# Kernel tuning notes

Measured on AMD Instinct MI355X. Metric: run time of the kernel, lower is better.

Reference implementation:

```python
import jax, jax.numpy as jnp
import numpy as np

B, D, N, H, K = 4, 1024, 4096, 16, 128
DH = D // H  # per-head dim (note: torch view splits D as (DH, H) in that order)
BN_EPS = 1e-3


def conv1(x, w, b):
    # 1x1 Conv1d == channel matmul: x [B,Cin,N], w [Cout,Cin], b [Cout]
    return jnp.einsum('oi,bin->bon', w, x) + b[None, :, None]


def setup_inputs() -> dict:
    key = jax.random.key(0)
    ks = jax.random.split(key, 16)
    s = 0.02
    proj_std = 1.0 / np.sqrt(K)  # init_() uniform(-1/sqrt(k), 1/sqrt(k))
    return {
        'x': jax.random.normal(ks[0], (B, D, N), jnp.float32),
        'source': jax.random.normal(ks[1], (B, D, N), jnp.float32),
        'to_q_w': jax.random.normal(ks[2], (D, D), jnp.float32) * s,
        'to_q_b': jnp.zeros((D,), jnp.float32),
        'to_k_w': jax.random.normal(ks[3], (D, D), jnp.float32) * s,
        'to_k_b': jnp.zeros((D,), jnp.float32),
        'proj_k': jax.random.uniform(ks[4], (N, K), jnp.float32, -proj_std, proj_std),
        'merge_w': jax.random.normal(ks[5], (D, D), jnp.float32) * s,
        'merge_b': jnp.zeros((D,), jnp.float32),
        'mlp_w1': jax.random.normal(ks[6], (2 * D, 2 * D), jnp.float32) * s,
        'mlp_b1': jnp.zeros((2 * D,), jnp.float32),
        'bn_gamma': jnp.ones((2 * D,), jnp.float32),
        'bn_beta': jnp.zeros((2 * D,), jnp.float32),
        'bn_mean': jnp.zeros((2 * D,), jnp.float32),
        'bn_var': jnp.ones((2 * D,), jnp.float32),
        'mlp_w2': jax.random.normal(ks[7], (D, 2 * D), jnp.float32) * s,
        'mlp_b2': jnp.zeros((D,), jnp.float32),
    }


def reference(x, source, to_q_w, to_q_b, to_k_w, to_k_b, proj_k, merge_w, merge_b,
              mlp_w1, mlp_b1, bn_gamma, bn_beta, bn_mean, bn_var, mlp_w2, mlp_b2):
    b = x.shape[0]
    q = conv1(x, to_q_w, to_q_b)          # [B,D,N]
    k = conv1(source, to_k_w, to_k_b)     # [B,D,M]
    v = k                                  # share_kv=True
    # Linformer sequence-length reduction: M -> K (proj_v == proj_k when shared)
    k = jnp.einsum('bdm,mk->bdk', k, proj_k)   # [B,D,K]
    v = jnp.einsum('bdm,mk->bdk', v, proj_k)   # [B,D,K]
    # torch .view(B, dim, heads, -1): channel axis split as (DH, H)
    qh = q.reshape(b, DH, H, N)
    kh = k.reshape(b, DH, H, K)
    vh = v.reshape(b, DH, H, K)
    scores = jnp.einsum('bdhn,bdhk->bhnk', qh, kh) / (DH ** 0.5)
    prob = jax.nn.softmax(scores, axis=-1)      # [B,H,N,K], small K
    msg = jnp.einsum('bhnk,bdhk->bdhn', prob, vh).reshape(b, D, N)
    msg = conv1(msg, merge_w, merge_b)
    # MLP([2D, 2D, D]): conv -> BN(eval, eps=1e-3) -> ReLU -> conv
    h = jnp.concatenate([x, msg], axis=1)       # [B,2D,N]
    h = conv1(h, mlp_w1, mlp_b1)
    h = bn_gamma[None, :, None] * (h - bn_mean[None, :, None]) \
        * jax.lax.rsqrt(bn_var + BN_EPS)[None, :, None] + bn_beta[None, :, None]
    h = jax.nn.relu(h)
    return conv1(h, mlp_w2, mlp_b2)             # [B,D,N]
```

## Files before the change

kernel.cpp:

```cpp
#include <hip/hip_runtime.h>
#include <stdint.h>

typedef __bf16 bf16x8 __attribute__((ext_vector_type(8)));
typedef float f32x4 __attribute__((ext_vector_type(4)));

__device__ __forceinline__ unsigned short f2bf(float f) {
    union { float f; uint32_t i; } v;
    v.f = f;
    uint32_t x = v.i;
    return (unsigned short)((x + 0x7FFFu + ((x >> 16) & 1u)) >> 16);
}

typedef __attribute__((address_space(3))) unsigned int lds_u32;
typedef __attribute__((address_space(1))) const unsigned int glob_u32;
__device__ __forceinline__ void gld16(const unsigned short* g, unsigned short* l) {
    __builtin_amdgcn_global_load_lds((glob_u32*)g, (lds_u32*)l, 16, 0, 0);
}

__global__ __launch_bounds__(256) void prep_weights(
    const float* __restrict__ Wq, const float* __restrict__ Wk,
    const float* __restrict__ Wm, const float* __restrict__ W1,
    const float* __restrict__ W2, const float* __restrict__ bq,
    const float* __restrict__ bk,
    unsigned short* __restrict__ wqb, unsigned short* __restrict__ wkb,
    unsigned short* __restrict__ wmb, unsigned short* __restrict__ w1b,
    unsigned short* __restrict__ w2b, float* __restrict__ bqp,
    float* __restrict__ bkp)
{
    const int b = blockIdx.x, t = threadIdx.x;
    if (b < 2048) {
        const float* in = (b < 1024) ? Wq : Wk;
        unsigned short* out = (b < 1024) ? wqb : wkb;
        const int i = ((b & 1023) * 256 + t) * 4;
        const int row = i >> 10, col = i & 1023;
        const float4 v = *(const float4*)(in + ((row & 63) * 16 + (row >> 6)) * 1024 + col);
        out[i + 0] = f2bf(v.x); out[i + 1] = f2bf(v.y);
        out[i + 2] = f2bf(v.z); out[i + 3] = f2bf(v.w);
    } else if (b < 3072) {
        const int i = ((b - 2048) * 256 + t) * 4;
        const int row = i >> 10, c0 = i & 1023;
        const float* r = Wm + (size_t)row * 1024;
#pragma unroll
        for (int j = 0; j < 4; ++j) {
            const int c = c0 + j;
            wmb[i + j] = f2bf(r[(c & 63) * 16 + (c >> 6)]);
        }
    } else if (b < 7168) {
        const int i = ((b - 3072) * 256 + t) * 4;
        const float4 v = *(const float4*)(W1 + i);
        w1b[i + 0] = f2bf(v.x); w1b[i + 1] = f2bf(v.y);
        w1b[i + 2] = f2bf(v.z); w1b[i + 3] = f2bf(v.w);
    } else if (b < 9216) {
        const int i = ((b - 7168) * 256 + t) * 4;
        const float4 v = *(const float4*)(W2 + i);
        w2b[i + 0] = f2bf(v.x); w2b[i + 1] = f2bf(v.y);
        w2b[i + 2] = f2bf(v.z); w2b[i + 3] = f2bf(v.w);
    } else {
        const int o = (b - 9216) * 256 + t;
        const int src = (o & 63) * 16 + (o >> 6);
        bqp[o] = bq[src];
        bkp[o] = bk[src];
    }
}

__global__ __launch_bounds__(256) void cvt_transpose(
    const float* __restrict__ in, unsigned short* __restrict__ out,
    int R, int C)
{
    __shared__ unsigned short tile[32][33];
    const size_t bo = (size_t)blockIdx.z * R * C;
    const int c0 = blockIdx.x * 32, r0 = blockIdx.y * 32;
    const int tx = threadIdx.x & 31, ty = threadIdx.x >> 5;
#pragma unroll
    for (int i = 0; i < 4; ++i)
        tile[ty + i * 8][tx] = f2bf(in[bo + (size_t)(r0 + ty + i * 8) * C + (c0 + tx)]);
    __syncthreads();
#pragma unroll
    for (int i = 0; i < 4; ++i)
        out[bo + (size_t)(c0 + ty + i * 8) * R + (r0 + tx)] = tile[tx][ty + i * 8];
}

__global__ __launch_bounds__(256) void cvt_transpose_xs(
    const float* __restrict__ x, const float* __restrict__ s,
    unsigned short* __restrict__ xt, unsigned short* __restrict__ st)
{
    __shared__ unsigned short tile[32][33];
    const int z = blockIdx.z;
    const float* in = (z < 4) ? x : s;
    unsigned short* out = (z < 4) ? xt : st;
    const size_t bo = (size_t)(z & 3) * 1024 * 4096;
    const int c0 = blockIdx.x * 32, r0 = blockIdx.y * 32;
    const int tx = threadIdx.x & 31, ty = threadIdx.x >> 5;
#pragma unroll
    for (int i = 0; i < 4; ++i)
        tile[ty + i * 8][tx] = f2bf(in[bo + (size_t)(r0 + ty + i * 8) * 4096 + (c0 + tx)]);
    __syncthreads();
#pragma unroll
    for (int i = 0; i < 4; ++i)
        out[bo + (size_t)(c0 + ty + i * 8) * 1024 + (r0 + tx)] = tile[tx][ty + i * 8];
}

template<int LDA, int LDB, int LDC, int KD, int SPLIT, bool CONCAT>
__global__ __launch_bounds__(256) void gemm_bt(
    const unsigned short* __restrict__ A,
    const unsigned short* __restrict__ A2, int K1,
    const unsigned short* __restrict__ BT,
    unsigned short* __restrict__ C, float* __restrict__ Cf,
    long long strideA, long long strideB, long long strideC,
    const float* __restrict__ bias_m,
    const float* __restrict__ bias_n,
    const float* __restrict__ bn_g,
    const float* __restrict__ bn_b,
    const float* __restrict__ bn_mu,
    const float* __restrict__ bn_var)
{
    constexpr int KPB = KD / SPLIT;
    __shared__ __align__(16) unsigned short As[128 * 64];
    __shared__ __align__(16) unsigned short Bs[128 * 64];

    const int z = blockIdx.z;
    const int batch = z / SPLIT;
    const int kbase = (z % SPLIT) * KPB;
    const int m0 = blockIdx.y * 128, n0 = blockIdx.x * 128;
    const unsigned short* Ab  = A + (size_t)batch * strideA;
    const unsigned short* A2b = CONCAT ? A2 + (size_t)batch * strideA
                                       : (const unsigned short*)0;
    const unsigned short* Bb = BT + (size_t)batch * strideB;

    const int t = threadIdx.x;
    const int lane = t & 63, wid = t >> 6;
    const int wm = wid >> 1, wn = wid & 1;
    const int r16 = lane & 15, quad = lane >> 4;

    f32x4 acc[4][4];
    const f32x4 zf = {0.f, 0.f, 0.f, 0.f};
#pragma unroll
    for (int i = 0; i < 4; ++i)
#pragma unroll
        for (int j = 0; j < 4; ++j) acc[i][j] = zf;

    for (int kt = kbase; kt < kbase + KPB; kt += 64) {
        const unsigned short* Asrc = Ab;
        int kk = kt;
        if (CONCAT && kt >= K1) { Asrc = A2b; kk = kt - K1; }
#pragma unroll
        for (int i = 0; i < 4; ++i) {
            const int p = i * 256 + t;
            const int row = p >> 3, slot = p & 7;
            const int kc = (slot ^ (row & 7)) * 8;
            gld16(&Asrc[(size_t)(m0 + row) * LDA + kk + kc], &As[p * 8]);
            gld16(&Bb[(size_t)(n0 + row) * LDB + kt + kc], &Bs[p * 8]);
        }
        __syncthreads();
#pragma unroll
        for (int s = 0; s < 2; ++s) {
            bf16x8 af[4], bfb[4];
#pragma unroll
            for (int i = 0; i < 4; ++i) {
                const int ra = wm * 64 + i * 16 + r16;
                const int rb = wn * 64 + i * 16 + r16;
                af[i]  = *(const bf16x8*)&As[(ra * 8 + ((s * 4 + quad) ^ (ra & 7))) * 8];
                bfb[i] = *(const bf16x8*)&Bs[(rb * 8 + ((s * 4 + quad) ^ (rb & 7))) * 8];
            }
#pragma unroll
            for (int mi = 0; mi < 4; ++mi)
#pragma unroll
                for (int ni = 0; ni < 4; ++ni)
                    acc[mi][ni] = __builtin_amdgcn_mfma_f32_16x16x32_bf16(
                        af[mi], bfb[ni], acc[mi][ni], 0, 0, 0);
        }
        __syncthreads();
    }

    unsigned short* Cb = C ? C + (size_t)z * strideC : (unsigned short*)0;
    float* Cfb = Cf ? Cf + (size_t)z * strideC : (float*)0;
    const bool has_bn = (bn_g != 0);
#pragma unroll
    for (int ni = 0; ni < 4; ++ni) {
        const int gn = n0 + wn * 64 + ni * 16 + r16;
        const float addn = bias_n ? bias_n[gn] : 0.f;
        float g = 1.f, bb = 0.f, mu = 0.f, rstd = 1.f;
        if (has_bn) {
            g = bn_g[gn]; bb = bn_b[gn]; mu = bn_mu[gn];
            rstd = rsqrtf(bn_var[gn] + 1e-3f);
        }
#pragma unroll
        for (int mi = 0; mi < 4; ++mi) {
            const int gm0 = m0 + wm * 64 + mi * 16 + quad * 4;
#pragma unroll
            for (int r = 0; r < 4; ++r) {
                float v = acc[mi][ni][r] + addn;
                if (bias_m) v += bias_m[gm0 + r];
                if (has_bn) { v = g * (v - mu) * rstd + bb; v = fmaxf(v, 0.f); }
                const size_t idx = (size_t)(gm0 + r) * LDC + gn;
                if (Cfb) Cfb[idx] = v;
                else     Cb[idx]  = f2bf(v);
            }
        }
    }
}

#define BAR   __builtin_amdgcn_s_barrier()
#define LGKM0 asm volatile("s_waitcnt lgkmcnt(0)" ::: "memory")
#define PRIO1 __builtin_amdgcn_s_setprio(1)
#define PRIO0 __builtin_amdgcn_s_setprio(0)

#define ST_A(dst, kt, i0, i1) do {                                          \
    const unsigned short* S_ = Ab; long long kk_ = (kt);                    \
    if (CONCAT && (kt) >= K1) { S_ = A2b; kk_ = (kt) - K1; }                \
    gld16(&S_[offA[i0] + kk_], (dst) + po[i0]);                             \
    gld16(&S_[offA[i1] + kk_], (dst) + po[i1]); } while (0)

#define ST_B(dst, kt, i0, i1) do {                                          \
    gld16(&Bb[offB[i0] + (kt)], (dst) + po[i0]);                            \
    gld16(&Bb[offB[i1] + (kt)], (dst) + po[i1]); } while (0)

#define RD_A(mh, AC) do {                                                   \
    _Pragma("unroll") for (int mi = 0; mi < 4; ++mi) {                      \
        const int ra = wm * 128 + (mh) * 64 + mi * 16 + r16;                \
        _Pragma("unroll") for (int ks = 0; ks < 2; ++ks) {                  \
            const int c_ = ks * 4 + quad;                                   \
            a[mi][ks] = *(const bf16x8*)&(AC)[(ra * 8 + (c_ ^ (ra & 7))) * 8]; \
        } } } while (0)

#define RD_B(np, BC) do {                                                   \
    _Pragma("unroll") for (int i = 0; i < 2; ++i) {                         \
        const int rb = wn * 64 + ((np) * 2 + i) * 16 + r16;                 \
        _Pragma("unroll") for (int ks = 0; ks < 2; ++ks) {                  \
            const int c_ = ks * 4 + quad;                                   \
            b[(np) * 2 + i][ks] = *(const bf16x8*)&(BC)[(rb * 8 + (c_ ^ (rb & 7))) * 8]; \
        } } } while (0)

#define MFMA_PH(mh, np) do {                                                \
    _Pragma("unroll") for (int mi = 0; mi < 4; ++mi)                        \
    _Pragma("unroll") for (int i = 0; i < 2; ++i)                           \
    _Pragma("unroll") for (int ks = 0; ks < 2; ++ks)                        \
        acc[(mh) * 4 + mi][(np) * 2 + i] =                                  \
            __builtin_amdgcn_mfma_f32_16x16x32_bf16(                        \
                a[mi][ks], b[(np) * 2 + i][ks],                             \
                acc[(mh) * 4 + mi][(np) * 2 + i], 0, 0, 0); } while (0)

#define TILE_BODY(XV, AC, BC, AN) do {                                      \
    const int kt1_ = ((XV) + 1) * 64, kt2_ = ((XV) + 2) * 64;               \
    const bool g1_ = ((XV) + 1) < nt, g2_ = ((XV) + 2) < nt;                \
       \
    RD_A(0, AC); RD_B(0, BC);                                               \
    if (g1_) ST_A(AN, kt1_, 1, 3);                                          \
    asm volatile("s_waitcnt lgkmcnt(8)" ::: "memory");                      \
    BAR; LGKM0; PRIO1; MFMA_PH(0, 0); PRIO0; BAR;                           \
                                  \
    RD_B(1, BC);                                                            \
    BAR; LGKM0; PRIO1; MFMA_PH(0, 1); PRIO0; BAR;                           \
         \
    RD_A(1, AC);                                                            \
    if (g2_) { ST_B(BC, kt2_, 0, 1); ST_B(BC, kt2_, 2, 3); }                \
    BAR; LGKM0; PRIO1; MFMA_PH(1, 1); PRIO0; BAR;                           \
             \
    if (g2_) { ST_A(AC, kt2_, 0, 2);                                        \
               asm volatile("s_waitcnt vmcnt(6)" ::: "memory"); }           \
    else     { asm volatile("s_waitcnt vmcnt(0)" ::: "memory"); }           \
    BAR; LGKM0; PRIO1; MFMA_PH(1, 0); PRIO0; BAR;                           \
} while (0)

template<int LDA, int LDB, int LDC, int KD, bool CONCAT>
__global__ __launch_bounds__(512, 2) void gemm256(
    const unsigned short* __restrict__ A,
    const unsigned short* __restrict__ A2, int K1,
    const unsigned short* __restrict__ BT,
    unsigned short* __restrict__ C, float* __restrict__ Cf,
    long long strideA, long long strideB, long long strideC,
    const float* __restrict__ bias_m,
    const float* __restrict__ bias_n,
    const float* __restrict__ bn_g,
    const float* __restrict__ bn_b,
    const float* __restrict__ bn_mu,
    const float* __restrict__ bn_var)
{
    static_assert(KD % 128 == 0, "nt must be even");
    constexpr int nt = KD / 64;
    constexpr int TILE = 256 * 64;
    __shared__ __align__(16) unsigned short As0[TILE];
    __shared__ __align__(16) unsigned short As1[TILE];
    __shared__ __align__(16) unsigned short Bs0[TILE];
    __shared__ __align__(16) unsigned short Bs1[TILE];

    const int batch = blockIdx.z;
    const int gx = gridDim.x;
    const int nwg = gx * gridDim.y;
    int flat = blockIdx.y * gx + blockIdx.x;
    flat = (flat & 7) * (nwg >> 3) + (flat >> 3);
    const int n0 = (flat % gx) * 256;
    const int m0 = (flat / gx) * 256;

    const unsigned short* Ab  = A + (size_t)batch * strideA;
    const unsigned short* A2b = CONCAT ? A2 + (size_t)batch * strideA
                                       : (const unsigned short*)0;
    const unsigned short* Bb  = BT + (size_t)batch * strideB;

    const int t = threadIdx.x;
    const int lane = t & 63, wid = t >> 6;
    const int wm = wid >> 2, wn = wid & 3;
    const int r16 = lane & 15, quad = lane >> 4;

    long long offA[4], offB[4];
    int po[4];
#pragma unroll
    for (int i = 0; i < 4; ++i) {
        const int p = i * 512 + t, row = p >> 3;
        const int kc = ((p & 7) ^ (row & 7)) * 8;
        po[i] = p * 8;
        offA[i] = (long long)(m0 + row) * LDA + kc;
        offB[i] = (long long)(n0 + row) * LDB + kc;
    }

    f32x4 acc[8][4];
    const f32x4 zf = {0.f, 0.f, 0.f, 0.f};
#pragma unroll
    for (int i = 0; i < 8; ++i)
#pragma unroll
        for (int j = 0; j < 4; ++j) acc[i][j] = zf;

    bf16x8 a[4][2], b[4][2];

    ST_A(As0, 0, 0, 2);
    ST_B(Bs0, 0, 0, 1);
    ST_B(Bs0, 0, 2, 3);
    ST_A(As0, 0, 1, 3);
    ST_B(Bs1, 64, 0, 1);
    ST_B(Bs1, 64, 2, 3);
    ST_A(As1, 64, 0, 2);
    asm volatile("s_waitcnt vmcnt(6)" ::: "memory");
    BAR;

#pragma unroll 1
    for (int X2 = 0; X2 < nt; X2 += 2) {
        TILE_BODY(X2,     As0, Bs0, As1);
        TILE_BODY(X2 + 1, As1, Bs1, As0);
    }

    unsigned short* Cb = C ? C + (size_t)batch * strideC : (unsigned short*)0;
    float* Cfb = Cf ? Cf + (size_t)batch * strideC : (float*)0;
    const bool has_bn = (bn_g != 0);

    float addn4[4], g4[4], b4[4], mu4[4], rs4[4];
#pragma unroll
    for (int ni = 0; ni < 4; ++ni) {
        const int gn = n0 + wn * 64 + ni * 16 + r16;
        addn4[ni] = bias_n ? bias_n[gn] : 0.f;
        if (has_bn) {
            g4[ni] = bn_g[gn]; b4[ni] = bn_b[gn]; mu4[ni] = bn_mu[gn];
            rs4[ni] = rsqrtf(bn_var[gn] + 1e-3f);
        }
    }
#pragma unroll
    for (int mi = 0; mi < 8; ++mi) {
        const int gm0 = m0 + wm * 128 + mi * 16 + quad * 4;
#pragma unroll
        for (int r = 0; r < 4; ++r) {
            const float bm_ = bias_m ? bias_m[gm0 + r] : 0.f;
            const size_t rowb = (size_t)(gm0 + r) * LDC + n0 + wn * 64 + r16;
#pragma unroll
            for (int ni = 0; ni < 4; ++ni) {
                float v = acc[mi][ni][r] + addn4[ni] + bm_;
                if (has_bn) {
                    v = g4[ni] * (v - mu4[ni]) * rs4[ni] + b4[ni];
                    v = fmaxf(v, 0.f);
                }
                if (Cfb) Cfb[rowb + ni * 16] = v;
                else     Cb[rowb + ni * 16]  = f2bf(v);
            }
        }
    }
}

#undef TILE_BODY
#undef MFMA_PH
#undef RD_B
#undef RD_A
#undef ST_B
#undef ST_A
#undef PRIO0
#undef PRIO1
#undef LGKM0
#undef BAR

__global__ __launch_bounds__(256) void reduce_kp(
    const float* __restrict__ acc, unsigned short* __restrict__ kpb)
{
    const int j = (blockIdx.x * 256 + threadIdx.x) * 4;
    const int b = j >> 17, jj = j & 131071;
    const float* base = acc + (size_t)b * 8 * 131072 + jj;
    float4 s = *(const float4*)base;
#pragma unroll
    for (int p = 1; p < 8; ++p) {
        const float4 v = *(const float4*)(base + (size_t)p * 131072);
        s.x += v.x; s.y += v.y; s.z += v.z; s.w += v.w;
    }
    kpb[j + 0] = f2bf(s.x); kpb[j + 1] = f2bf(s.y);
    kpb[j + 2] = f2bf(s.z); kpb[j + 3] = f2bf(s.w);
}

__global__ __launch_bounds__(256) void attn_fused(
    const unsigned short* __restrict__ qT,
    const unsigned short* __restrict__ kp,
    unsigned short* __restrict__ msgT)
{
    constexpr int QS = 72, KS = 72, VS = 136, PS = 136;
    __shared__ __align__(16) unsigned short QKP[128 * QS + 128 * KS];
    __shared__ __align__(16) unsigned short Vs[64 * VS];
    unsigned short* Qs = QKP;
    unsigned short* Ks = QKP + 128 * QS;
    unsigned short* Ps = QKP;

    const int t = threadIdx.x;
    const int lane = t & 63, w = t >> 6;
    const int r16 = lane & 15, quad = lane >> 4;
    const int h = blockIdx.y, n0 = blockIdx.x * 128;
    const size_t b = blockIdx.z;

    const unsigned short* qbase = qT + (b * 4096 + n0) * 1024 + h * 64;
    const unsigned short* kbase = kp + (b * 1024 + h * 64) * 128;

#pragma unroll
    for (int i = 0; i < 4; ++i) {
        const int c = i * 256 + t;
        const int n = c >> 3, dh0 = (c & 7) * 8;
        *(int4*)&Qs[n * QS + dh0] = *(const int4*)&qbase[(size_t)n * 1024 + dh0];
    }
#pragma unroll
    for (int i = 0; i < 4; ++i) {
        const int c = i * 256 + t;
        const int kkq = c & 3, dh = (c >> 2) & 63, kkh = c >> 8;
        const int kk0 = kkh * 32 + kkq * 8;
        const bf16x8 v = *(const bf16x8*)&kbase[(size_t)dh * 128 + kk0];
        *(bf16x8*)&Vs[dh * VS + kk0] = v;
        const unsigned short* vs = (const unsigned short*)&v;
#pragma unroll
        for (int j = 0; j < 8; ++j) Ks[(kk0 + j) * KS + dh] = vs[j];
    }
    __syncthreads();

    f32x4 S[2][8];
    const f32x4 zf = {0.f, 0.f, 0.f, 0.f};
#pragma unroll
    for (int mi = 0; mi < 2; ++mi)
#pragma unroll
        for (int ni = 0; ni < 8; ++ni) S[mi][ni] = zf;

    bf16x8 aq[2][2];
#pragma unroll
    for (int mi = 0; mi < 2; ++mi)
#pragma unroll
        for (int ks = 0; ks < 2; ++ks)
            aq[mi][ks] = *(const bf16x8*)&Qs[(w * 32 + mi * 16 + r16) * QS + ks * 32 + quad * 8];
#pragma unroll
    for (int ni = 0; ni < 8; ++ni) {
        const bf16x8 b0 = *(const bf16x8*)&Ks[(ni * 16 + r16) * KS + quad * 8];
        const bf16x8 b1 = *(const bf16x8*)&Ks[(ni * 16 + r16) * KS + 32 + quad * 8];
#pragma unroll
        for (int mi = 0; mi < 2; ++mi) {
            S[mi][ni] = __builtin_amdgcn_mfma_f32_16x16x32_bf16(aq[mi][0], b0, S[mi][ni], 0, 0, 0);
            S[mi][ni] = __builtin_amdgcn_mfma_f32_16x16x32_bf16(aq[mi][1], b1, S[mi][ni], 0, 0, 0);
        }
    }

    __syncthreads();

    float linv[2][4];
#pragma unroll
    for (int mi = 0; mi < 2; ++mi) {
        float e[8][4];
        float rs0 = 0.f, rs1 = 0.f, rs2 = 0.f, rs3 = 0.f;
#pragma unroll
        for (int ni = 0; ni < 8; ++ni) {
            e[ni][0] = __expf(S[mi][ni][0] * 0.125f); rs0 += e[ni][0];
            e[ni][1] = __expf(S[mi][ni][1] * 0.125f); rs1 += e[ni][1];
            e[ni][2] = __expf(S[mi][ni][2] * 0.125f); rs2 += e[ni][2];
            e[ni][3] = __expf(S[mi][ni][3] * 0.125f); rs3 += e[ni][3];
        }
        float rs[4] = {rs0, rs1, rs2, rs3};
#pragma unroll
        for (int r = 0; r < 4; ++r) {
            float s = rs[r];
            s += __shfl_xor(s, 1); s += __shfl_xor(s, 2);
            s += __shfl_xor(s, 4); s += __shfl_xor(s, 8);
            linv[mi][r] = 1.f / s;
        }
#pragma unroll
        for (int ni = 0; ni < 8; ++ni)
#pragma unroll
            for (int r = 0; r < 4; ++r)
                Ps[(w * 32 + mi * 16 + quad * 4 + r) * PS + ni * 16 + r16] = f2bf(e[ni][r]);
    }
    __syncthreads();

    f32x4 O[2][4];
#pragma unroll
    for (int mi = 0; mi < 2; ++mi)
#pragma unroll
        for (int ni = 0; ni < 4; ++ni) O[mi][ni] = zf;

    bf16x8 ap[2][4];
#pragma unroll
    for (int mi = 0; mi < 2; ++mi)
#pragma unroll
        for (int ks = 0; ks < 4; ++ks)
            ap[mi][ks] = *(const bf16x8*)&Ps[(w * 32 + mi * 16 + r16) * PS + ks * 32 + quad * 8];
#pragma unroll
    for (int ni = 0; ni < 4; ++ni)
#pragma unroll
        for (int ks = 0; ks < 4; ++ks) {
            const bf16x8 bv = *(const bf16x8*)&Vs[(ni * 16 + r16) * VS + ks * 32 + quad * 8];
#pragma unroll
            for (int mi = 0; mi < 2; ++mi)
                O[mi][ni] = __builtin_amdgcn_mfma_f32_16x16x32_bf16(ap[mi][ks], bv, O[mi][ni], 0, 0, 0);
        }

    unsigned short* ob = msgT + (b * 4096 + n0) * 1024 + h * 64;
#pragma unroll
    for (int mi = 0; mi < 2; ++mi)
#pragma unroll
        for (int ni = 0; ni < 4; ++ni)
#pragma unroll
            for (int r = 0; r < 4; ++r)
                ob[(size_t)(w * 32 + mi * 16 + quad * 4 + r) * 1024 + ni * 16 + r16] =
                    f2bf(O[mi][ni][r] * linv[mi][r]);
}

extern "C" void kernel_launch(void* const* d_in, const int* in_sizes, int n_in,
                              void* d_out, int out_size, void* d_ws, size_t ws_size,
                              hipStream_t stream)
{
    (void)in_sizes; (void)n_in; (void)out_size; (void)ws_size;
    const float* x    = (const float*)d_in[0];
    const float* srcp = (const float*)d_in[1];
    const float* Wq   = (const float*)d_in[2];
    const float* bq   = (const float*)d_in[3];
    const float* Wk   = (const float*)d_in[4];
    const float* bk   = (const float*)d_in[5];
    const float* proj = (const float*)d_in[6];
    const float* Wm   = (const float*)d_in[7];
    const float* bm   = (const float*)d_in[8];
    const float* W1   = (const float*)d_in[9];
    const float* b1   = (const float*)d_in[10];
    const float* gam  = (const float*)d_in[11];
    const float* bet  = (const float*)d_in[12];
    const float* mu   = (const float*)d_in[13];
    const float* var  = (const float*)d_in[14];
    const float* W2   = (const float*)d_in[15];
    const float* b2   = (const float*)d_in[16];
    float* out = (float*)d_out;
    unsigned short* ws = (unsigned short*)d_ws;

    const long long E = 16777216LL;
    unsigned short* xt  = ws;
    unsigned short* st  = xt + E;
    unsigned short* qt  = st + E;
    unsigned short* kc  = qt + E;
    unsigned short* ht  = kc + E;
    unsigned short* pT  = ht + 2 * E;
    unsigned short* kpb = pT + 524288;
    unsigned short* wqb = kpb + 524288;
    unsigned short* wkb = wqb + 1048576;
    unsigned short* wmb = wkb + 1048576;
    unsigned short* w1b = wmb + 1048576;
    unsigned short* w2b = w1b + 4194304;
    float* bqp = (float*)(w2b + 2097152);
    float* bkp = bqp + 1024;
    float* kpacc = (float*)ht;

    cvt_transpose_xs<<<dim3(128, 32, 8), 256, 0, stream>>>(x, srcp, xt, st);
    cvt_transpose<<<dim3(4, 128, 1), 256, 0, stream>>>(proj, pT, 4096, 128);
    prep_weights<<<9220, 256, 0, stream>>>(Wq, Wk, Wm, W1, W2, bq, bk,
                                           wqb, wkb, wmb, w1b, w2b, bqp, bkp);

    gemm256<1024, 1024, 1024, 1024, false><<<dim3(4, 16, 4), 512, 0, stream>>>(
        xt, nullptr, 1024, wqb, qt, nullptr,
        4096LL * 1024, 0LL, 4096LL * 1024, nullptr, bqp,
        nullptr, nullptr, nullptr, nullptr);
    gemm256<1024, 1024, 4096, 1024, false><<<dim3(16, 4, 4), 512, 0, stream>>>(
        wkb, nullptr, 1024, st, kc, nullptr,
        0LL, 4096LL * 1024, 1024LL * 4096, bkp, nullptr,
        nullptr, nullptr, nullptr, nullptr);
    gemm_bt<4096, 4096, 128, 4096, 8, false><<<dim3(1, 8, 32), 256, 0, stream>>>(
        kc, nullptr, 4096, pT, nullptr, kpacc,
        1024LL * 4096, 0LL, 1024LL * 128, nullptr, nullptr,
        nullptr, nullptr, nullptr, nullptr);
    reduce_kp<<<512, 256, 0, stream>>>(kpacc, kpb);
    attn_fused<<<dim3(32, 16, 4), 256, 0, stream>>>(qt, kpb, qt);
    gemm256<1024, 1024, 1024, 1024, false><<<dim3(4, 16, 4), 512, 0, stream>>>(
        qt, nullptr, 1024, wmb, st, nullptr,
        4096LL * 1024, 0LL, 4096LL * 1024, nullptr, bm,
        nullptr, nullptr, nullptr, nullptr);
    gemm256<1024, 2048, 2048, 2048, true><<<dim3(8, 16, 4), 512, 0, stream>>>(
        xt, st, 1024, w1b, ht, nullptr,
        4096LL * 1024, 0LL, 4096LL * 2048, nullptr, b1,
        gam, bet, mu, var);
    gemm256<2048, 2048, 4096, 2048, false><<<dim3(16, 4, 4), 512, 0, stream>>>(
        w2b, nullptr, 2048, ht, nullptr, out,
        0LL, 4096LL * 2048, 1024LL * 4096, b2, nullptr,
        nullptr, nullptr, nullptr, nullptr);
}
```

Before: 619.7 us.

## Restructure GEMM pipeline to prefetch one tile ahead in two MFMA phases

The GEMM main loop previously ran four barrier-separated MFMA phases per tile and kept loads two tiles ahead, staggering A and B stores across phases. It now uses two phases per tile, each doing twice the MFMA work, and issues all global-to-LDS loads for only the next tile. The prologue loads just the first tile. This halves the number of barriers per tile and simplifies the schedule, at the cost of a shallower prefetch distance, which may expose more global memory latency.

```diff
diff --git a/kernel.cpp b/kernel.cpp
--- a/kernel.cpp
+++ b/kernel.cpp
@@ -240,26 +240,22 @@
                 a[mi][ks], b[(np) * 2 + i][ks],                             \
                 acc[(mh) * 4 + mi][(np) * 2 + i], 0, 0, 0); } while (0)
 
-#define TILE_BODY(XV, AC, BC, AN) do {                                      \
-    const int kt1_ = ((XV) + 1) * 64, kt2_ = ((XV) + 2) * 64;               \
-    const bool g1_ = ((XV) + 1) < nt, g2_ = ((XV) + 2) < nt;                \
-       \
-    RD_A(0, AC); RD_B(0, BC);                                               \
-    if (g1_) ST_A(AN, kt1_, 1, 3);                                          \
-    asm volatile("s_waitcnt lgkmcnt(8)" ::: "memory");                      \
-    BAR; LGKM0; PRIO1; MFMA_PH(0, 0); PRIO0; BAR;                           \
-                                  \
-    RD_B(1, BC);                                                            \
-    BAR; LGKM0; PRIO1; MFMA_PH(0, 1); PRIO0; BAR;                           \
-         \
-    RD_A(1, AC);                                                            \
-    if (g2_) { ST_B(BC, kt2_, 0, 1); ST_B(BC, kt2_, 2, 3); }                \
-    BAR; LGKM0; PRIO1; MFMA_PH(1, 1); PRIO0; BAR;                           \
-             \
-    if (g2_) { ST_A(AC, kt2_, 0, 2);                                        \
+#define TILE_BODY(XV, AC, BC, AN, BN_) do {                                 \
+    const int kt1_ = ((XV) + 1) * 64;                                       \
+    const bool g1_ = ((XV) + 1) < nt;                                       \
+          \
+    RD_A(0, AC); RD_B(0, BC); RD_B(1, BC);                                  \
+    if (g1_) { ST_A(AN, kt1_, 0, 2); ST_B(BN_, kt1_, 0, 1);                 \
+               ST_B(BN_, kt1_, 2, 3);                                       \
                asm volatile("s_waitcnt vmcnt(6)" ::: "memory"); }           \
     else     { asm volatile("s_waitcnt vmcnt(0)" ::: "memory"); }           \
-    BAR; LGKM0; PRIO1; MFMA_PH(1, 0); PRIO0; BAR;                           \
+    BAR; LGKM0; PRIO1; MFMA_PH(0, 0); MFMA_PH(0, 1); PRIO0; BAR;            \
+                      \
+    RD_A(1, AC);                                                            \
+    if (g1_) { ST_A(AN, kt1_, 1, 3);                                        \
+               asm volatile("s_waitcnt vmcnt(2)" ::: "memory"); }           \
+    else     { asm volatile("s_waitcnt vmcnt(0)" ::: "memory"); }           \
+    BAR; LGKM0; PRIO1; MFMA_PH(1, 1); MFMA_PH(1, 0); PRIO0; BAR;            \
 } while (0)
 
 template<int LDA, int LDB, int LDC, int KD, bool CONCAT>
@@ -326,16 +322,13 @@
     ST_B(Bs0, 0, 0, 1);
     ST_B(Bs0, 0, 2, 3);
     ST_A(As0, 0, 1, 3);
-    ST_B(Bs1, 64, 0, 1);
-    ST_B(Bs1, 64, 2, 3);
-    ST_A(As1, 64, 0, 2);
-    asm volatile("s_waitcnt vmcnt(6)" ::: "memory");
+    asm volatile("s_waitcnt vmcnt(2)" ::: "memory");
     BAR;
 
 #pragma unroll 1
     for (int X2 = 0; X2 < nt; X2 += 2) {
-        TILE_BODY(X2,     As0, Bs0, As1);
-        TILE_BODY(X2 + 1, As1, Bs1, As0);
+        TILE_BODY(X2,     As0, Bs0, As1, Bs1);
+        TILE_BODY(X2 + 1, As1, Bs1, As0, Bs0);
     }
 
     unsigned short* Cb = C ? C + (size_t)batch * strideC : (unsigned short*)0;
```

Result: no change. 618.4 us (-0.2%).
